# Kernel tuning notes

Measured on AMD Instinct MI355X. Metric: run time of the kernel, lower is better.

The kernel has to match this reference:

```python
import math
import jax, jax.numpy as jnp
import numpy as np

B, N, C = 4, 2048, 256
KMAX, RATIO, ITERS, H = 1024, 12.0, 3, 4
TAU, SIG_FLOOR, INIT_SIG_MIX, INIT_OFF, JIT = 1.0, 0.03, 0.1, 0.5, 1e-6
W_KL, W_ENT, W_OCC, W_COL = 0.05, 0.0, 0.5, 0.1
K_USE = min(max(1, math.ceil(N / RATIO)), KMAX)  # 171
EPS = 1e-8


def _sym(M):
    return 0.5 * (M + jnp.swapaxes(M, -1, -2))


def _l2n(x):
    return x / jnp.maximum(jnp.linalg.norm(x, axis=-1, keepdims=True), 1e-12)


def _ln(x, g, b):
    m = x.mean(-1, keepdims=True)
    v = ((x - m) ** 2).mean(-1, keepdims=True)
    return (x - m) / jnp.sqrt(v + 1e-5) * g + b


def setup_inputs():
    key = jax.random.key(0)
    ks = jax.random.split(key, 16)
    s = jax.random.normal(ks[0], (B, N, C), jnp.float32)
    mu = jax.random.normal(ks[1], (B, N, 3), jnp.float32)
    # per-point SPD covariances (Sigma must be PSD for the overlap solve)
    L = jax.random.normal(ks[2], (B, N, 3, 3), jnp.float32) * 0.3
    Sigma = L @ jnp.swapaxes(L, -1, -2) + 0.05 * jnp.eye(3, dtype=jnp.float32)
    mask = jnp.ones((B, N), jnp.float32)
    lim = 1.0 / math.sqrt(C)
    u = lambda k, sh: jax.random.uniform(k, sh, jnp.float32, -lim, lim)
    return dict(
        s=s, mu=mu, Sigma=Sigma, mask=mask,
        slot_embed_pool=jax.random.normal(ks[3], (KMAX, C), jnp.float32) * 0.02,
        geo_offsets_pool=jax.random.normal(ks[4], (KMAX, 3), jnp.float32) * 0.5,
        gating_W=u(ks[5], (C, C)), proj_q_W=u(ks[6], (C, C)), proj_k_W=u(ks[7], (C, C)),
        gru_w_ih=u(ks[8], (3 * C, C)), gru_w_hh=u(ks[9], (3 * C, C)),
        gru_b_ih=u(ks[10], (3 * C,)), gru_b_hh=u(ks[11], (3 * C,)),
        ln_g=jnp.ones((C,), jnp.float32), ln_b=jnp.zeros((C,), jnp.float32),
        mlp_w1=u(ks[12], (4 * C, C)), mlp_b1=u(ks[13], (4 * C,)),
        mlp_w2=u(ks[14], (C, 4 * C)), mlp_b2=u(ks[15], (C,)),
        w_geo=jnp.float32(1.0),
        geo_scale_raw=jnp.full((H,), -4.0, jnp.float32),
        geo_bias=jnp.full((H,), -6.0, jnp.float32),
    )


def _forward(s, mu, Sigma, mask, slot_embed_pool, geo_offsets_pool, gating_W,
             proj_q_W, proj_k_W, gru_w_ih, gru_w_hh, gru_b_ih, gru_b_hh,
             ln_g, ln_b, mlp_w1, mlp_b1, mlp_w2, mlp_b2,
             w_geo, geo_scale_raw, geo_bias):
    I3 = jnp.eye(3, dtype=s.dtype)
    m1 = mask[:, :, None]                    # [B,N,1]
    cnt = jnp.maximum(mask.sum(1), EPS)      # [B]

    # ---- slot selection (eval mode: no gate noise, rand_slots=0) ----
    s_global = (s * m1).sum(1) / cnt[:, None]
    q = _l2n(s_global @ gating_W.T)
    kn = _l2n(slot_embed_pool)
    scores = q @ kn.T                        # [B,KMAX]
    idx = jax.lax.top_k(scores, K_USE)[1]    # [B,K]
    slots = slot_embed_pool[idx]             # [B,K,C]
    geo_off = geo_offsets_pool[idx]          # [B,K,3]

    # ---- masked mean/std of mu ----
    mean = (mu * m1).sum(1) / cnt[:, None]   # [B,3]
    dm = mu - mean[:, None, :]
    cov = jnp.einsum('bni,bnj->bij', dm * m1, dm) / cnt[:, None, None]
    cov = _sym(cov)
    std = jnp.sqrt(jnp.maximum(jnp.diagonal(cov, axis1=-2, axis2=-1), EPS))
    std = jnp.maximum(std, SIG_FLOOR)
    mu_k = mean[:, None, :] + geo_off * (INIT_OFF * std[:, None, :])

    Sig_avg = _sym((Sigma * m1[..., None]).sum(1) / cnt[:, None, None])
    Sig_k = jnp.broadcast_to(Sig_avg[:, None] * INIT_SIG_MIX, (B, K_USE, 3, 3))
    Sig_k = Sig_k + (SIG_FLOOR ** 2) * I3 + JIT * I3

    k_sem = s @ proj_k_W.T                   # [B,N,C]
    a_h = jax.nn.softplus(geo_scale_raw)     # [H]
    A = None
    for _ in range(ITERS):
        q_sem = slots @ proj_q_W.T           # [B,K,C]
        logits_sem = jnp.einsum('bnc,bkc->bnk', k_sem, q_sem) / math.sqrt(C)
        delta = mu[:, :, None, :] - mu_k[:, None, :, :]       # [B,N,K,3]
        sig_sum = Sigma[:, :, None] + Sig_k[:, None]          # [B,N,K,3,3]
        sol = jnp.linalg.solve(sig_sum, delta[..., None])[..., 0]
        maha = (delta * sol).sum(-1)
        logdet = jnp.linalg.slogdet(sig_sum)[1]
        G = -0.5 * (maha + logdet)                            # [B,N,K]
        geo = (a_h[None, :, None, None] * G[:, None] + geo_bias[None, :, None, None]).sum(1)
        logits = (logits_sem + w_geo * geo) / max(TAU, 1e-6)
        logits = jnp.where(m1 < 0.5, -1e9, logits)
        A = jax.nn.softmax(logits, axis=-1) * m1              # [B,N,K]
        # moment-matching merge (A already mask-weighted; matches torch A*mask)
        occ = jnp.maximum(A.sum(1), EPS)                      # [B,K]
        mu_k = jnp.einsum('bnk,bni->bki', A, mu) / occ[..., None]
        d = mu[:, :, None, :] - mu_k[:, None, :, :]
        outer = d[..., :, None] * d[..., None, :]             # [B,N,K,3,3]
        Sig_k = (jnp.einsum('bnk,bnij->bkij', A, Sigma)
                 + jnp.einsum('bnk,bnkij->bkij', A, outer)) / occ[:, :, None, None]
        Sig_k = _sym(Sig_k) + max(JIT, 1e-6) * I3
        dg = jnp.diagonal(Sig_k, axis1=-2, axis2=-1)
        dg_f = jnp.maximum(dg, SIG_FLOOR ** 2)
        Sig_k = Sig_k - I3 * dg[..., None, :] + I3 * dg_f[..., None, :]
        Sig_k = _sym(Sig_k) + JIT * I3
        denom = jnp.maximum(A.sum(1), 1e-8)
        slot_in = jnp.einsum('bnk,bnc->bkc', A, s) / denom[..., None]
        # GRU cell
        x = slot_in.reshape(-1, C)
        h = slots.reshape(-1, C)
        gi = x @ gru_w_ih.T + gru_b_ih
        gh = h @ gru_w_hh.T + gru_b_hh
        r = jax.nn.sigmoid(gi[:, :C] + gh[:, :C])
        z = jax.nn.sigmoid(gi[:, C:2 * C] + gh[:, C:2 * C])
        n = jnp.tanh(gi[:, 2 * C:] + r * gh[:, 2 * C:])
        slots = ((1.0 - z) * n + z * h).reshape(B, K_USE, C)
        xm = _ln(slots, ln_g, ln_b)
        slots = slots + (jax.nn.gelu(xm @ mlp_w1.T + mlp_b1, approximate=False) @ mlp_w2.T + mlp_b2)

    # ---- losses ----
    hist = jnp.zeros((KMAX,), jnp.float32).at[idx.reshape(-1)].add(1.0)
    p = hist / jnp.maximum(hist.sum(), 1.0)
    pc = jnp.maximum(p, 1e-8)
    usage_kl = (pc * (jnp.log(pc) - math.log(1.0 / KMAX))).sum()
    usage_neg_ent = (pc * jnp.log(pc)).sum()
    occ2 = (A * m1).sum(1)
    occ2 = occ2 / jnp.maximum(occ2.sum(-1, keepdims=True), 1e-8)
    occ_mse = ((occ2 - 1.0 / K_USE) ** 2).mean()
    X = jnp.swapaxes(A * m1, 1, 2)           # [B,K,N]
    Xn = X / jnp.maximum(jnp.linalg.norm(X, axis=-1, keepdims=True), 1e-8)
    Gm = jnp.einsum('bkn,bln->bkl', Xn, Xn)
    eyeK = jnp.eye(K_USE, dtype=A.dtype)[None]
    off = (Gm - eyeK) * (1.0 - eyeK)
    col = (off ** 2).mean()
    total = W_KL * usage_kl + W_ENT * usage_neg_ent + W_OCC * occ_mse + W_COL * col
    return (A, slots, mu_k, Sig_k, idx, usage_kl, usage_neg_ent, occ_mse, col, total)


def reference(s, mu, Sigma, mask, slot_embed_pool, geo_offsets_pool, gating_W,
              proj_q_W, proj_k_W, gru_w_ih, gru_w_hh, gru_b_ih, gru_b_hh,
              ln_g, ln_b, mlp_w1, mlp_b1, mlp_w2, mlp_b2,
              w_geo, geo_scale_raw, geo_bias):
    return _forward(s, mu, Sigma, mask, slot_embed_pool, geo_offsets_pool, gating_W,
                    proj_q_W, proj_k_W, gru_w_ih, gru_w_hh, gru_b_ih, gru_b_hh,
                    ln_g, ln_b, mlp_w1, mlp_b1, mlp_w2, mlp_b2,
                    w_geo, geo_scale_raw, geo_bias)
```

## Files before the change

kernel.cpp:

```cpp
#include <hip/hip_runtime.h>
#include <math.h>

#define B_ 4
#define N_ 2048
#define C_ 256
#define KMAX_ 1024
#define KU_ 171
#define BK_ 684
#define ITERS_ 3
#define H_ 4
#define EPS_ 1e-8f
#define SIGF_ 0.03f
#define JIT_ 1e-6f
#define LOGKMAX_ 6.93147180559945f

#define WS_CNT 0
#define WS_MUS 4
#define WS_MOS 16
#define WS_SGS 40
#define WS_COLACC 100
#define WS_SSUM 128
#define WS_STATS_BYTES (1152*4)
#define WS_MEAN 1152
#define WS_STD 1164
#define WS_SIGAVG 1176
#define WS_IDXI 1216
#define WS_KSEM 1920
#define WS_QSEM (WS_KSEM+2097152)
#define WS_OCC  (WS_QSEM+175104)
#define WS_PART (WS_OCC+704)
#define WS_W2P  WS_PART
#define WS_GBUF (WS_PART+1400832)
#define WS_ATA  WS_GBUF
#define WS_SNEW (WS_GBUF+700416)
#define WS_HID  (WS_SNEW+175104)
#define WS_ACPART (WS_HID+700416)
#define WS_QV   (WS_ACPART+28160)
#define WS_SCORE (WS_QV+1024)

#define O_A 0
#define O_SLOTS 1400832
#define O_MUK   1575936
#define O_SIGK  1577988
#define O_IDX   1584144
#define O_KL    1584828
#define O_ENT   1584829
#define O_OCC   1584830
#define O_COL   1584831
#define O_TOT   1584832

__device__ __forceinline__ float wred(float v) {
  #pragma unroll
  for (int i = 32; i; i >>= 1) v += __shfl_xor(v, i);
  return v;
}
__device__ __forceinline__ float wmax(float v) {
  #pragma unroll
  for (int i = 32; i; i >>= 1) v = fmaxf(v, __shfl_xor(v, i));
  return v;
}

__device__ __forceinline__ float blk_red(float v, float* red, int t) {
  red[t] = v; __syncthreads();
  #pragma unroll
  for (int s = 128; s > 0; s >>= 1) {
    if (t < s) red[t] += red[t + s];
    __syncthreads();
  }
  float r = red[0]; __syncthreads();
  return r;
}

__global__ __launch_bounds__(256) void k_stats(const float* __restrict__ s,
    const float* __restrict__ mu, const float* __restrict__ Sigma,
    const float* __restrict__ mask, float* __restrict__ ws) {
  int blk = blockIdx.x; int b = blk / 8; int nc = blk % 8; int t = threadIdx.x;
  int n = nc * 256 + t;
  float m = mask[b * N_ + n];
  const float* mun = mu + ((size_t)(b * N_ + n)) * 3;
  float m0 = mun[0], m1v = mun[1], m2 = mun[2];
  const float* sgn = Sigma + ((size_t)(b * N_ + n)) * 9;
  float sg[9];
  #pragma unroll
  for (int j = 0; j < 9; j++) sg[j] = sgn[j];
  int lane = t & 63;
  float vals[19];
  vals[0] = m; vals[1] = m * m0; vals[2] = m * m1v; vals[3] = m * m2;
  vals[4] = m * m0 * m0; vals[5] = m * m0 * m1v; vals[6] = m * m0 * m2;
  vals[7] = m * m1v * m1v; vals[8] = m * m1v * m2; vals[9] = m * m2 * m2;
  #pragma unroll
  for (int j = 0; j < 9; j++) vals[10 + j] = m * sg[j];
  #pragma unroll
  for (int j = 0; j < 19; j++) {
    float v = wred(vals[j]);
    if (lane == 0) {
      int base = (j == 0) ? WS_CNT + b : (j < 4 ? WS_MUS + b * 3 + (j - 1)
                 : (j < 10 ? WS_MOS + b * 6 + (j - 4) : WS_SGS + b * 9 + (j - 10)));
      atomicAdd(ws + base, v);
    }
  }
  const float* sb = s + ((size_t)b * N_ + nc * 256) * C_;
  const float* mk = mask + b * N_ + nc * 256;
  float sa = 0.f;
  #pragma unroll 4
  for (int nn = 0; nn < 256; nn++) sa += mk[nn] * sb[(size_t)nn * C_ + t];
  atomicAdd(ws + WS_SSUM + b * C_ + t, sa);
}

__global__ __launch_bounds__(256) void k_qv(float* __restrict__ ws,
    const float* __restrict__ gW, float* __restrict__ qv_o) {
  int b = blockIdx.x, t = threadIdx.x;
  __shared__ float sb[C_];
  __shared__ float rv[256];
  sb[t] = ws[WS_SSUM + b * C_ + t];
  __syncthreads();
  if (blockIdx.x == 0 && t < B_) {
    int bb = t;
    float cnt = fmaxf(ws[WS_CNT + bb], EPS_);
    float me[3];
    #pragma unroll
    for (int i = 0; i < 3; i++) { me[i] = ws[WS_MUS + bb * 3 + i] / cnt; ws[WS_MEAN + bb * 3 + i] = me[i]; }
    const int dg[3] = {0, 3, 5};
    #pragma unroll
    for (int i = 0; i < 3; i++) {
      float cov = ws[WS_MOS + bb * 6 + dg[i]] / cnt - me[i] * me[i];
      ws[WS_STD + bb * 3 + i] = fmaxf(sqrtf(fmaxf(cov, EPS_)), SIGF_);
    }
    #pragma unroll
    for (int i = 0; i < 3; i++)
      #pragma unroll
      for (int j = 0; j < 3; j++)
        ws[WS_SIGAVG + bb * 9 + i * 3 + j] =
            0.5f * (ws[WS_SGS + bb * 9 + i * 3 + j] + ws[WS_SGS + bb * 9 + j * 3 + i]) / cnt;
  }
  const float4* g4 = (const float4*)(gW + (size_t)t * C_);
  float qr = 0.f;
  #pragma unroll 4
  for (int c4 = 0; c4 < 64; c4++) {
    float4 g = g4[c4];
    qr += sb[c4 * 4] * g.x + sb[c4 * 4 + 1] * g.y + sb[c4 * 4 + 2] * g.z + sb[c4 * 4 + 3] * g.w;
  }
  float n2 = blk_red(qr * qr, rv, t);
  qv_o[b * C_ + t] = qr / fmaxf(sqrtf(n2), 1e-12f);
}

__global__ __launch_bounds__(256) void k_score(const float* __restrict__ qv,
    const float* __restrict__ pool, float* __restrict__ score) {
  int blk = blockIdx.x; int b = blk >> 4; int pc = blk & 15;
  int t = threadIdx.x; int row = pc * 64 + (t >> 2); int q = t & 3;
  __shared__ float qs[C_];
  qs[t] = qv[b * C_ + t];
  __syncthreads();
  const float4* p4 = (const float4*)(pool + (size_t)row * C_ + q * 64);
  float d = 0.f, p2 = 0.f;
  #pragma unroll
  for (int i = 0; i < 16; i++) {
    float4 pv = p4[i];
    int c = q * 64 + i * 4;
    d += qs[c] * pv.x + qs[c + 1] * pv.y + qs[c + 2] * pv.z + qs[c + 3] * pv.w;
    p2 += pv.x * pv.x + pv.y * pv.y + pv.z * pv.z + pv.w * pv.w;
  }
  d += __shfl_xor(d, 1); d += __shfl_xor(d, 2);
  p2 += __shfl_xor(p2, 1); p2 += __shfl_xor(p2, 2);
  if (q == 0) score[b * KMAX_ + row] = d / fmaxf(sqrtf(p2), 1e-12f);
}

__global__ __launch_bounds__(256) void k_sort(const float* __restrict__ score,
    int* __restrict__ idx_o, float* __restrict__ idxf_o) {
  int b = blockIdx.x, t = threadIdx.x;
  __shared__ float val[KMAX_]; __shared__ int id[KMAX_];
  for (int j = t; j < KMAX_; j += 256) { val[j] = score[b * KMAX_ + j]; id[j] = j; }
  __syncthreads();
  for (int kk = 2; kk <= KMAX_; kk <<= 1) {
    for (int j = kk >> 1; j > 0; j >>= 1) {
      for (int i = t; i < KMAX_; i += 256) {
        int ix = i ^ j;
        if (ix > i) {
          float va = val[i], vb = val[ix]; int ia = id[i], ib = id[ix];
          bool bBeforeA = (vb > va) || (vb == va && ib < ia);
          bool up = ((i & kk) == 0);
          if (up == bBeforeA) {
            val[i] = vb; val[ix] = va; id[i] = ib; id[ix] = ia;
          }
        }
      }
      __syncthreads();
    }
  }
  if (t < KU_) {
    idx_o[b * KU_ + t] = id[t];
    idxf_o[b * KU_ + t] = (float)id[t];
  }
}

__global__ __launch_bounds__(256) void k_init(const int* __restrict__ idx,
    const float* __restrict__ pool, const float* __restrict__ geop,
    const float* __restrict__ ws, float* __restrict__ slots,
    float* __restrict__ mu_k, float* __restrict__ sig_k) {
  int blk = blockIdx.x; int b = blk / KU_, k = blk % KU_; int t = threadIdx.x;
  int j = idx[b * KU_ + k];
  slots[((size_t)(b * KU_ + k)) * C_ + t] = pool[(size_t)j * C_ + t];
  if (t < 3) {
    mu_k[(b * KU_ + k) * 3 + t] = ws[WS_MEAN + b * 3 + t] + geop[j * 3 + t] * (0.5f * ws[WS_STD + b * 3 + t]);
  }
  if (t < 9) {
    float v = ws[WS_SIGAVG + b * 9 + t] * 0.1f;
    if (t == 0 || t == 4 || t == 8) v += SIGF_ * SIGF_ + JIT_;
    sig_k[((size_t)(b * KU_ + k)) * 9 + t] = v;
  }
}

template<int ROWS>
__global__ __launch_bounds__(256) void k_gemm_plain(const float* __restrict__ in,
    const float* __restrict__ W, float* __restrict__ out, int IN, int OUT, float scale) {
  extern __shared__ float sm[];
  int t = threadIdx.x; int r0 = blockIdx.x * ROWS;
  int C4 = IN >> 2;
  for (int i = t; i < ROWS * C4; i += 256) {
    int rr = i / C4;
    ((float4*)sm)[i] = ((const float4*)(in + (size_t)(r0 + rr) * IN))[i - rr * C4];
  }
  __syncthreads();
  const float4* W4 = (const float4*)(W + (size_t)t * IN);
  const float4* sm4 = (const float4*)sm;
  float acc[ROWS];
  #pragma unroll
  for (int a = 0; a < ROWS; a++) acc[a] = 0.f;
  for (int c4 = 0; c4 < C4; c4++) {
    float4 wv = W4[c4];
    #pragma unroll
    for (int a = 0; a < ROWS; a++) {
      float4 sv = sm4[a * C4 + c4];
      acc[a] += sv.x * wv.x + sv.y * wv.y + sv.z * wv.z + sv.w * wv.w;
    }
  }
  #pragma unroll
  for (int a = 0; a < ROWS; a++)
    out[(size_t)(r0 + a) * OUT + t] = acc[a] * scale;
}

#define LG_R 8
__global__ __launch_bounds__(256) void k_lgsm(const float* __restrict__ ksem,
    const float* __restrict__ qsem, const float* __restrict__ mu,
    const float* __restrict__ Sigma, const float* __restrict__ mask,
    const float* __restrict__ mu_k, const float* __restrict__ sig_k,
    const float* __restrict__ wgeo, const float* __restrict__ gsr,
    const float* __restrict__ gbias, float* __restrict__ A) {
  __shared__ float ksm[LG_R * C_];
  __shared__ float Asm[LG_R][172];
  __shared__ float muk[KU_ * 3];
  __shared__ float sgk[KU_ * 6];
  __shared__ float rowd[LG_R][10];
  int blk = blockIdx.x; int b = blk / (N_ / LG_R); int nt = blk % (N_ / LG_R);
  int t = threadIdx.x; int r0 = nt * LG_R;
  for (int i = t; i < LG_R * (C_ >> 2); i += 256) {
    int rr = i >> 6;
    ((float4*)ksm)[i] = ((const float4*)(ksem + ((size_t)(b * N_ + r0 + rr)) * C_))[i & 63];
  }
  for (int i = t; i < KU_ * 3; i += 256) muk[i] = mu_k[(size_t)b * KU_ * 3 + i];
  for (int i = t; i < KU_ * 6; i += 256) {
    int k = i / 6, c = i % 6;
    const int map[6] = {0, 1, 2, 4, 5, 8};
    sgk[i] = sig_k[((size_t)(b * KU_ + k)) * 9 + map[c]];
  }
  if (t < LG_R * 10) {
    int rr = t / 10, c = t % 10;
    int n = r0 + rr;
    float v;
    if (c == 0) v = mask[b * N_ + n];
    else if (c < 4) v = mu[((size_t)(b * N_ + n)) * 3 + (c - 1)];
    else {
      const int map[6] = {0, 1, 2, 4, 5, 8};
      v = Sigma[((size_t)(b * N_ + n)) * 9 + map[c - 4]];
    }
    rowd[rr][c] = v;
  }
  __syncthreads();
  if (t < KU_) {
    const float4* q4 = (const float4*)(qsem + ((size_t)(b * KU_ + t)) * C_);
    const float4* sm4 = (const float4*)ksm;
    float acc[LG_R];
    #pragma unroll
    for (int a = 0; a < LG_R; a++) acc[a] = 0.f;
    for (int c4 = 0; c4 < 64; c4++) {
      float4 qv = q4[c4];
      #pragma unroll
      for (int a = 0; a < LG_R; a++) {
        float4 sv = sm4[a * 64 + c4];
        acc[a] += sv.x * qv.x + sv.y * qv.y + sv.z * qv.z + sv.w * qv.w;
      }
    }
    float ah = 0.f, bs = 0.f;
    #pragma unroll
    for (int h = 0; h < H_; h++) {
      float x = gsr[h];
      ah += fmaxf(x, 0.f) + log1pf(expf(-fabsf(x)));
      bs += gbias[h];
    }
    float wg = wgeo[0];
    float mk0 = muk[t * 3], mk1 = muk[t * 3 + 1], mk2 = muk[t * 3 + 2];
    float k00 = sgk[t * 6], k01 = sgk[t * 6 + 1], k02 = sgk[t * 6 + 2];
    float k11 = sgk[t * 6 + 3], k12 = sgk[t * 6 + 4], k22 = sgk[t * 6 + 5];
    #pragma unroll
    for (int a = 0; a < LG_R; a++) {
      float m = rowd[a][0];
      float d0 = rowd[a][1] - mk0, d1 = rowd[a][2] - mk1, d2 = rowd[a][3] - mk2;
      float s00 = rowd[a][4] + k00, s01 = rowd[a][5] + k01, s02 = rowd[a][6] + k02;
      float s11 = rowd[a][7] + k11, s12 = rowd[a][8] + k12, s22 = rowd[a][9] + k22;
      float c00 = s11 * s22 - s12 * s12;
      float c01 = s02 * s12 - s01 * s22;
      float c02 = s01 * s12 - s02 * s11;
      float det = s00 * c00 + s01 * c01 + s02 * c02;
      float c11 = s00 * s22 - s02 * s02;
      float c12 = s01 * s02 - s00 * s12;
      float c22 = s00 * s11 - s01 * s01;
      float inv = 1.0f / det;
      float x0 = (c00 * d0 + c01 * d1 + c02 * d2) * inv;
      float x1 = (c01 * d0 + c11 * d1 + c12 * d2) * inv;
      float x2 = (c02 * d0 + c12 * d1 + c22 * d2) * inv;
      float maha = d0 * x0 + d1 * x1 + d2 * x2;
      float logdet = logf(fmaxf(det, 1e-30f));
      float G = -0.5f * (maha + logdet);
      float l = acc[a] * 0.0625f + wg * (ah * G + bs);
      if (m < 0.5f) l = -1e9f;
      Asm[a][t] = l;
    }
  }
  __syncthreads();
  int w = t >> 6, lane = t & 63;
  #pragma unroll
  for (int q = 0; q < 2; q++) {
    int a = w * 2 + q;
    float v0 = (lane < KU_) ? Asm[a][lane] : -INFINITY;
    float v1 = (lane + 64 < KU_) ? Asm[a][lane + 64] : -INFINITY;
    float v2 = (lane + 128 < KU_) ? Asm[a][lane + 128] : -INFINITY;
    float mx = wmax(fmaxf(v0, fmaxf(v1, v2)));
    float e0 = (lane < KU_) ? expf(v0 - mx) : 0.f;
    float e1 = (lane + 64 < KU_) ? expf(v1 - mx) : 0.f;
    float e2 = (lane + 128 < KU_) ? expf(v2 - mx) : 0.f;
    float ss = wred(e0 + e1 + e2);
    float scale = rowd[a][0] / ss;
    if (lane < KU_) Asm[a][lane] = e0 * scale;
    if (lane + 64 < KU_) Asm[a][lane + 64] = e1 * scale;
    if (lane + 128 < KU_) Asm[a][lane + 128] = e2 * scale;
  }
  __syncthreads();
  for (int i = t; i < LG_R * KU_; i += 256) {
    int a = i / KU_, k = i - a * KU_;
    A[((size_t)(b * N_ + r0 + a)) * KU_ + k] = Asm[a][k];
  }
}

#define AC_NC 4
__global__ __launch_bounds__(256) void k_amoms(const float* __restrict__ A,
    const float* __restrict__ mu, const float* __restrict__ Sigma,
    const float* __restrict__ s, float* __restrict__ acpart,
    float* __restrict__ atpart) {
  __shared__ float shm[1024];
  __shared__ float red2[4][16][10];
  int t = threadIdx.x;
  if (blockIdx.x < 176) {
    int blk = blockIdx.x;
    int nc = blk & 3; int tmp = blk >> 2; int kt = tmp % 11; int b = tmp / 11;
    int nn = t >> 4; int kk = t & 15;
    int k = kt * 16 + kk;
    float S[10];
    #pragma unroll
    for (int i = 0; i < 10; i++) S[i] = 0.f;
    float (*rowd)[10] = (float(*)[10])shm;
    const int NCH = N_ / AC_NC;
    for (int n0 = nc * NCH; n0 < nc * NCH + NCH; n0 += 16) {
      __syncthreads();
      if (t < 144) {
        int rr = t / 9, c = t % 9;
        int n = n0 + rr;
        float v;
        if (c < 3) v = mu[((size_t)(b * N_ + n)) * 3 + c];
        else {
          const int map[6] = {0, 1, 2, 4, 5, 8};
          v = Sigma[((size_t)(b * N_ + n)) * 9 + map[c - 3]];
        }
        rowd[rr][c] = v;
      }
      float a = (k < KU_) ? A[((size_t)(b * N_ + n0 + nn)) * KU_ + k] : 0.f;
      __syncthreads();
      float m0 = rowd[nn][0], m1 = rowd[nn][1], m2 = rowd[nn][2];
      float g0 = rowd[nn][3], g1 = rowd[nn][4], g2 = rowd[nn][5];
      float g4 = rowd[nn][6], g5 = rowd[nn][7], g8 = rowd[nn][8];
      S[0] += a; S[1] += a * m0; S[2] += a * m1; S[3] += a * m2;
      S[4] += a * (g0 + m0 * m0); S[5] += a * (g1 + m0 * m1); S[6] += a * (g2 + m0 * m2);
      S[7] += a * (g4 + m1 * m1); S[8] += a * (g5 + m1 * m2); S[9] += a * (g8 + m2 * m2);
    }
    #pragma unroll
    for (int i = 0; i < 10; i++) { S[i] += __shfl_xor(S[i], 16); S[i] += __shfl_xor(S[i], 32); }
    int w = t >> 6, lane = t & 63;
    if (lane < 16) {
      #pragma unroll
      for (int i = 0; i < 10; i++) red2[w][lane][i] = S[i];
    }
    __syncthreads();
    if (t < 160) {
      int k2 = t / 10, i = t % 10;
      float v = red2[0][k2][i] + red2[1][k2][i] + red2[2][k2][i] + red2[3][k2][i];
      acpart[(((size_t)nc * B_ + b) * 176 + kt * 16 + k2) * 10 + i] = v;
    }
  } else {
    int blk = blockIdx.x - 176;
    int nc = blk & 7; int tmp = blk >> 3; int kt = tmp % 11; int b = tmp / 11;
    int k0 = kt * 16;
    float* Ach = shm;
    float acc[16];
    #pragma unroll
    for (int j = 0; j < 16; j++) acc[j] = 0.f;
    for (int n0 = nc * 256; n0 < nc * 256 + 256; n0 += 64) {
      __syncthreads();
      for (int i = t; i < 64 * 16; i += 256) {
        int nn = i >> 4, kk = i & 15; int k = k0 + kk;
        Ach[i] = (k < KU_) ? A[((size_t)(b * N_ + n0 + nn)) * KU_ + k] : 0.f;
      }
      __syncthreads();
      for (int nn = 0; nn < 64; nn++) {
        float xv = s[((size_t)(b * N_ + n0 + nn)) * C_ + t];
        #pragma unroll
        for (int j = 0; j < 16; j++) acc[j] += Ach[(nn << 4) + j] * xv;
      }
    }
    #pragma unroll
    for (int j = 0; j < 16; j++) {
      int k = k0 + j;
      if (k < KU_) atpart[((size_t)nc * (B_ * BK_ / 4) + b * KU_ + k) * C_ + t] = acc[j];
    }
  }
}

__global__ __launch_bounds__(256) void k_gg(const float* __restrict__ atpart,
    const float* __restrict__ acpart, const float* __restrict__ slots,
    const float* __restrict__ wih, const float* __restrict__ bih,
    const float* __restrict__ whh, const float* __restrict__ bhh,
    float* __restrict__ gbuf, float* __restrict__ occ,
    float* __restrict__ mu_k, float* __restrict__ sig_k) {
  int t = threadIdx.x;
  if (blockIdx.x >= 86) {
    if (blockIdx.y != 0) return;
    int i = (blockIdx.x - 86) * 256 + t;
    if (i >= B_ * KU_) return;
    int b = i / KU_, k = i % KU_;
    float p[10];
    #pragma unroll
    for (int j = 0; j < 10; j++) {
      float v = 0.f;
      #pragma unroll
      for (int nc = 0; nc < AC_NC; nc++)
        v += acpart[(((size_t)nc * B_ + b) * 176 + k) * 10 + j];
      p[j] = v;
    }
    float o = p[0];
    occ[b * KU_ + k] = o;
    float oc = fmaxf(o, EPS_);
    float s1x = p[1], s1y = p[2], s1z = p[3];
    float q0 = s1x / oc, q1 = s1y / oc, q2 = s1z / oc;
    mu_k[(b * KU_ + k) * 3 + 0] = q0;
    mu_k[(b * KU_ + k) * 3 + 1] = q1;
    mu_k[(b * KU_ + k) * 3 + 2] = q2;
    float v00 = (p[4] - 2.f * q0 * s1x + o * q0 * q0) / oc + JIT_;
    float v01 = (p[5] - q0 * s1y - s1x * q1 + o * q0 * q1) / oc;
    float v02 = (p[6] - q0 * s1z - s1x * q2 + o * q0 * q2) / oc;
    float v11 = (p[7] - 2.f * q1 * s1y + o * q1 * q1) / oc + JIT_;
    float v12 = (p[8] - q1 * s1z - s1y * q2 + o * q1 * q2) / oc;
    float v22 = (p[9] - 2.f * q2 * s1z + o * q2 * q2) / oc + JIT_;
    v00 = fmaxf(v00, SIGF_ * SIGF_) + JIT_;
    v11 = fmaxf(v11, SIGF_ * SIGF_) + JIT_;
    v22 = fmaxf(v22, SIGF_ * SIGF_) + JIT_;
    float* po = sig_k + ((size_t)(b * KU_ + k)) * 9;
    po[0] = v00; po[1] = v01; po[2] = v02;
    po[3] = v01; po[4] = v11; po[5] = v12;
    po[6] = v02; po[7] = v12; po[8] = v22;
    return;
  }
  int p = blockIdx.y; int r0 = blockIdx.x * 8;
  __shared__ float sx[8 * C_];
  __shared__ float sh[8 * C_];
  __shared__ float socc[8];
  bool needx = (p < 3), needh = (p != 2);
  if (t < 8) {
    int r = r0 + t;
    float o = 0.f;
    if (r < BK_) {
      int b = r / KU_, k = r % KU_;
      #pragma unroll
      for (int nc = 0; nc < AC_NC; nc++)
        o += acpart[(((size_t)nc * B_ + b) * 176 + k) * 10];
    }
    socc[t] = fmaxf(o, 1e-8f);
  }
  __syncthreads();
  for (int i = t; i < 8 * C_; i += 256) {
    int rr = i >> 8, c = i & 255;
    int r = r0 + rr;
    if (r < BK_) {
      if (needx) {
        float v = 0.f;
        #pragma unroll
        for (int nc = 0; nc < 8; nc++) v += atpart[((size_t)nc * BK_ + r) * C_ + c];
        sx[i] = v / socc[rr];
      }
      if (needh) sh[i] = slots[(size_t)r * C_ + c];
    } else {
      if (needx) sx[i] = 0.f;
      if (needh) sh[i] = 0.f;
    }
  }
  __syncthreads();
  int grow = (p >= 2) ? 512 + t : p * 256 + t;
  float acc[8];
  #pragma unroll
  for (int a = 0; a < 8; a++) acc[a] = 0.f;
  const float4* sx4 = (const float4*)sx;
  const float4* sh4 = (const float4*)sh;
  if (p < 2) {
    const float4* wi = (const float4*)(wih + (size_t)grow * C_);
    const float4* wh = (const float4*)(whh + (size_t)grow * C_);
    for (int c4 = 0; c4 < 64; c4++) {
      float4 a1 = wi[c4], a2 = wh[c4];
      #pragma unroll
      for (int a = 0; a < 8; a++) {
        float4 xv = sx4[a * 64 + c4], hv = sh4[a * 64 + c4];
        acc[a] += xv.x * a1.x + xv.y * a1.y + xv.z * a1.z + xv.w * a1.w
                + hv.x * a2.x + hv.y * a2.y + hv.z * a2.z + hv.w * a2.w;
      }
    }
  } else if (p == 2) {
    const float4* wi = (const float4*)(wih + (size_t)grow * C_);
    for (int c4 = 0; c4 < 64; c4++) {
      float4 a1 = wi[c4];
      #pragma unroll
      for (int a = 0; a < 8; a++) {
        float4 xv = sx4[a * 64 + c4];
        acc[a] += xv.x * a1.x + xv.y * a1.y + xv.z * a1.z + xv.w * a1.w;
      }
    }
  } else {
    const float4* wh = (const float4*)(whh + (size_t)grow * C_);
    for (int c4 = 0; c4 < 64; c4++) {
      float4 a2 = wh[c4];
      #pragma unroll
      for (int a = 0; a < 8; a++) {
        float4 hv = sh4[a * 64 + c4];
        acc[a] += hv.x * a2.x + hv.y * a2.y + hv.z * a2.z + hv.w * a2.w;
      }
    }
  }
  float bias = (p < 2) ? (bih[grow] + bhh[grow]) : ((p == 2) ? bih[grow] : bhh[grow]);
  #pragma unroll
  for (int a = 0; a < 8; a++) {
    int r = r0 + a;
    if (r < BK_) gbuf[((size_t)p * BK_ + r) * C_ + t] = acc[a] + bias;
  }
}

__global__ __launch_bounds__(256) void k_w1ln(const float* __restrict__ gbuf,
    const float* __restrict__ slots, const float* __restrict__ lng,
    const float* __restrict__ lnb, const float* __restrict__ w1p,
    const float* __restrict__ b1p, float* __restrict__ snew,
    float* __restrict__ hid) {
  int r0 = blockIdx.x * 4; int t = threadIdx.x; int oc = blockIdx.y * 256 + t;
  __shared__ float ssn[4 * C_];
  __shared__ float sxm[4 * C_];
  bool wr = (blockIdx.y == 0);
  for (int i = t; i < 4 * C_; i += 256) {
    int rr = i >> 8, c = i & 255;
    int r = r0 + rr;
    float gr = gbuf[((size_t)0 * BK_ + r) * C_ + c];
    float gz = gbuf[((size_t)1 * BK_ + r) * C_ + c];
    float gi = gbuf[((size_t)2 * BK_ + r) * C_ + c];
    float gh = gbuf[((size_t)3 * BK_ + r) * C_ + c];
    float rg = 1.f / (1.f + expf(-gr));
    float z = 1.f / (1.f + expf(-gz));
    float n = tanhf(gi + rg * gh);
    float h = slots[(size_t)r * C_ + c];
    float sn = (1.f - z) * n + z * h;
    ssn[i] = sn;
    if (wr) snew[(size_t)r * C_ + c] = sn;
  }
// ... 94 lines not shown
  int nc = blk & 7; int tmp = blk >> 3; int kt = tmp % 11; int b = tmp / 11;
  int t = threadIdx.x; int k0 = kt * 16;
  __shared__ float Ach[64 * 16];
  float acc[16];
  #pragma unroll
  for (int j = 0; j < 16; j++) acc[j] = 0.f;
  for (int n0 = nc * 256; n0 < nc * 256 + 256; n0 += 64) {
    __syncthreads();
    for (int i = t; i < 64 * 16; i += 256) {
      int nn = i >> 4, kk = i & 15; int k = k0 + kk;
      Ach[i] = (k < KU_) ? A[((size_t)(b * N_ + n0 + nn)) * KU_ + k] : 0.f;
    }
    __syncthreads();
    if (t < NX) {
      for (int nn = 0; nn < 64; nn++) {
        float xv = X[((size_t)(b * N_ + n0 + nn)) * NX + t];
        #pragma unroll
        for (int j = 0; j < 16; j++) acc[j] += Ach[(nn << 4) + j] * xv;
      }
    }
  }
  if (t < NX) {
    #pragma unroll
    for (int j = 0; j < 16; j++) {
      int k = k0 + j;
      if (k < KU_) atomicAdd(&out[((size_t)(b * KU_ + k)) * NX + t], acc[j]);
    }
  }
}

__global__ __launch_bounds__(256) void k_histocc(const int* __restrict__ idx,
    const float* __restrict__ occ, float* __restrict__ okl,
    float* __restrict__ oent, float* __restrict__ oocc) {
  int t = threadIdx.x;
  __shared__ float buf[KMAX_];
  __shared__ float red[256];
  if (blockIdx.x == 0) {
    for (int i = t; i < KMAX_; i += 256) buf[i] = 0.f;
    __syncthreads();
    for (int i = t; i < B_ * KU_; i += 256) atomicAdd(&buf[idx[i]], 1.0f);
    __syncthreads();
    float kl = 0.f, ent = 0.f;
    const float tot = (float)(B_ * KU_);
    for (int i = t; i < KMAX_; i += 256) {
      float pc = fmaxf(buf[i] / tot, 1e-8f);
      float lp = logf(pc);
      kl += pc * (lp + LOGKMAX_);
      ent += pc * lp;
    }
    kl = blk_red(kl, red, t); ent = blk_red(ent, red, t);
    if (t == 0) { okl[0] = kl; oent[0] = ent; }
  } else {
    for (int i = t; i < B_ * KU_; i += 256) buf[i] = occ[i];
    __syncthreads();
    __shared__ float bsum[B_];
    for (int b = 0; b < B_; b++) {
      float s = 0.f;
      for (int i = t; i < KU_; i += 256) s += buf[b * KU_ + i];
      s = blk_red(s, red, t);
      if (t == 0) bsum[b] = fmaxf(s, 1e-8f);
      __syncthreads();
    }
    float acc = 0.f;
    const float invK = 1.0f / (float)KU_;
    for (int i = t; i < B_ * KU_; i += 256) {
      int b = i / KU_;
      float v = buf[i] / bsum[b] - invK;
      acc += v * v;
    }
    acc = blk_red(acc, red, t);
    if (t == 0) oocc[0] = acc / (float)(B_ * KU_);
  }
}

__global__ __launch_bounds__(256) void k_colpart(const float* __restrict__ AtA,
    float* __restrict__ colacc) {
  int blk = blockIdx.x; int b = blk / KU_, k = blk % KU_; int t = threadIdx.x;
  float acc = 0.f;
  if (t < KU_ && t != k) {
    float dk = AtA[((size_t)(b * KU_ + k)) * KU_ + k];
    float dt = AtA[((size_t)(b * KU_ + t)) * KU_ + t];
    float v  = AtA[((size_t)(b * KU_ + k)) * KU_ + t];
    float gm = v / (fmaxf(sqrtf(dk), 1e-8f) * fmaxf(sqrtf(dt), 1e-8f));
    acc = gm * gm;
  }
  float v = wred(acc);
  __shared__ float p[4];
  if ((t & 63) == 0) p[t >> 6] = v;
  __syncthreads();
  if (t == 0) atomicAdd(colacc, p[0] + p[1] + p[2] + p[3]);
}

__global__ void k_colfin(const float* __restrict__ colacc,
    const float* __restrict__ okl, const float* __restrict__ oent,
    const float* __restrict__ oocc, float* __restrict__ ocol, float* __restrict__ otot) {
  float col = colacc[0] / (float)(B_ * KU_ * KU_);
  ocol[0] = col;
  otot[0] = 0.05f * okl[0] + 0.0f * oent[0] + 0.5f * oocc[0] + 0.1f * col;
}

extern "C" void kernel_launch(void* const* d_in, const int* in_sizes, int n_in,
                              void* d_out_v, int out_size, void* d_ws, size_t ws_size,
                              hipStream_t stream) {
  const float* s     = (const float*)d_in[0];
  const float* mu    = (const float*)d_in[1];
  const float* Sigma = (const float*)d_in[2];
  const float* mask  = (const float*)d_in[3];
  const float* pool  = (const float*)d_in[4];
  const float* geop  = (const float*)d_in[5];
  const float* gW    = (const float*)d_in[6];
  const float* qW    = (const float*)d_in[7];
  const float* kW    = (const float*)d_in[8];
  const float* wih   = (const float*)d_in[9];
  const float* whh   = (const float*)d_in[10];
  const float* bih   = (const float*)d_in[11];
  const float* bhh   = (const float*)d_in[12];
  const float* lng   = (const float*)d_in[13];
  const float* lnb   = (const float*)d_in[14];
  const float* w1    = (const float*)d_in[15];
  const float* b1    = (const float*)d_in[16];
  const float* w2    = (const float*)d_in[17];
  const float* b2    = (const float*)d_in[18];
  const float* wgeo  = (const float*)d_in[19];
  const float* gsr   = (const float*)d_in[20];
  const float* gbias = (const float*)d_in[21];

  float* out = (float*)d_out_v;
  float* A     = out + O_A;
  float* slots = out + O_SLOTS;
  float* muk   = out + O_MUK;
  float* sigk  = out + O_SIGK;
  float* idxf  = out + O_IDX;
  float* okl   = out + O_KL;
  float* oent  = out + O_ENT;
  float* oocc  = out + O_OCC;
  float* ocol  = out + O_COL;
  float* otot  = out + O_TOT;

  float* ws = (float*)d_ws;
  int*   idxi   = (int*)(ws + WS_IDXI);
  float* ksem   = ws + WS_KSEM;
  float* qsem   = ws + WS_QSEM;
  float* occ    = ws + WS_OCC;
  float* atpart = ws + WS_PART;
  float* gbuf   = ws + WS_GBUF;
  float* snew   = ws + WS_SNEW;
  float* hid    = ws + WS_HID;
  float* w2part = ws + WS_W2P;
  float* acpart = ws + WS_ACPART;
  float* ata    = ws + WS_ATA;
  float* colacc = ws + WS_COLACC;

  hipMemsetAsync(ws, 0, WS_STATS_BYTES, stream);
  k_stats<<<B_ * 8, 256, 0, stream>>>(s, mu, Sigma, mask, ws);
  k_qv<<<B_, 256, 0, stream>>>(ws, gW, ws + WS_QV);
  k_score<<<B_ * 16, 256, 0, stream>>>(ws + WS_QV, pool, ws + WS_SCORE);
  k_sort<<<B_, 256, 0, stream>>>(ws + WS_SCORE, idxi, idxf);
  k_init<<<B_ * KU_, 256, 0, stream>>>(idxi, pool, geop, ws, slots, muk, sigk);

  k_gemm_plain<8><<<1024, 256, 8 * C_ * 4, stream>>>(s, kW, ksem, C_, C_, 1.0f);
  k_gemm_plain<4><<<171, 256, 4 * C_ * 4, stream>>>(slots, qW, qsem, C_, C_, 1.0f);

  for (int it = 0; it < ITERS_; ++it) {
    k_lgsm<<<B_ * (N_ / LG_R), 256, 0, stream>>>(ksem, qsem, mu, Sigma, mask,
                                                 muk, sigk, wgeo, gsr, gbias, A);
    k_amoms<<<176 + 352, 256, 0, stream>>>(A, mu, Sigma, s, acpart, atpart);
    k_gg<<<dim3(89, 4), 256, 0, stream>>>(atpart, acpart, slots, wih, bih, whh, bhh,
                                          gbuf, occ, muk, sigk);
    k_w1ln<<<dim3(171, 4), 256, 0, stream>>>(gbuf, slots, lng, lnb, w1, b1, snew, hid);
    k_w2p<<<dim3(171, 4), 256, 0, stream>>>(hid, w2, w2part);
    k_qsemf<<<171, 256, 0, stream>>>(snew, w2part, b2, qW, slots, qsem);
  }

  hipMemsetAsync(ata, 0, (size_t)B_ * KU_ * KU_ * 4, stream);
  k_atn<<<B_ * 11 * 8, 256, 0, stream>>>(A, A, ata, KU_);
  k_colpart<<<B_ * KU_, 256, 0, stream>>>(ata, colacc);
  k_histocc<<<2, 256, 0, stream>>>(idxi, occ, okl, oent, oocc);
  k_colfin<<<1, 1, 0, stream>>>(colacc, okl, oent, oocc, ocol, otot);
}
```

Measured before the change: 786.5 us.

## Register-tile projection GEMMs and logit kernel; split stats into separate kernels

Replaces the per-thread single-output-column GEMM with a 32-row register-tiled kernel where each thread computes 8 rows by 4 columns. The logit/softmax kernel now handles 32 rows per block, with each thread covering 8 rows by 3 slots. Before, only 171 of 256 threads did work in that kernel. The s-row summation moves out of the stats kernel into a wider grid so it no longer runs serially over 256 rows per thread. The aim is to cut weight reloads and raise utilisation, at the cost of more registers and shared memory and fewer blocks for the logit kernel.

```diff
diff --git a/kernel.cpp b/kernel.cpp
--- a/kernel.cpp
+++ b/kernel.cpp
@@ -71,9 +71,9 @@
   return r;
 }
 
-__global__ __launch_bounds__(256) void k_stats(const float* __restrict__ s,
-    const float* __restrict__ mu, const float* __restrict__ Sigma,
-    const float* __restrict__ mask, float* __restrict__ ws) {
+__global__ __launch_bounds__(256) void k_mom(const float* __restrict__ mu,
+    const float* __restrict__ Sigma, const float* __restrict__ mask,
+    float* __restrict__ ws) {
   int blk = blockIdx.x; int b = blk / 8; int nc = blk % 8; int t = threadIdx.x;
   int n = nc * 256 + t;
   float m = mask[b * N_ + n];
@@ -99,11 +99,16 @@
       atomicAdd(ws + base, v);
     }
   }
-  const float* sb = s + ((size_t)b * N_ + nc * 256) * C_;
-  const float* mk = mask + b * N_ + nc * 256;
+}
+
+__global__ __launch_bounds__(256) void k_ssum(const float* __restrict__ s,
+    const float* __restrict__ mask, float* __restrict__ ws) {
+  int blk = blockIdx.x; int b = blk / 64; int nc = blk % 64; int t = threadIdx.x;
+  const float* sb = s + ((size_t)b * N_ + nc * 32) * C_;
+  const float* mk = mask + b * N_ + nc * 32;
   float sa = 0.f;
-  #pragma unroll 4
-  for (int nn = 0; nn < 256; nn++) sa += mk[nn] * sb[(size_t)nn * C_ + t];
+  #pragma unroll 8
+  for (int nn = 0; nn < 32; nn++) sa += mk[nn] * sb[(size_t)nn * C_ + t];
   atomicAdd(ws + WS_SSUM + b * C_ + t, sa);
 }
 
@@ -210,50 +215,66 @@
   }
 }
 
-template<int ROWS>
-__global__ __launch_bounds__(256) void k_gemm_plain(const float* __restrict__ in,
-    const float* __restrict__ W, float* __restrict__ out, int IN, int OUT, float scale) {
-  extern __shared__ float sm[];
-  int t = threadIdx.x; int r0 = blockIdx.x * ROWS;
-  int C4 = IN >> 2;
-  for (int i = t; i < ROWS * C4; i += 256) {
-    int rr = i / C4;
-    ((float4*)sm)[i] = ((const float4*)(in + (size_t)(r0 + rr) * IN))[i - rr * C4];
-  }
-  __syncthreads();
-  const float4* W4 = (const float4*)(W + (size_t)t * IN);
+__global__ __launch_bounds__(256) void k_gemm32(const float* __restrict__ in,
+    const float* __restrict__ W, float* __restrict__ out, int R) {
+  __shared__ float sm[32 * C_];
+  int t = threadIdx.x; int r0 = blockIdx.x * 32;
+  for (int i = t; i < 32 * 64; i += 256) {
+    int rr = i >> 6; int r = r0 + rr;
+    float4 v = {0.f, 0.f, 0.f, 0.f};
+    if (r < R) v = ((const float4*)(in + (size_t)r * C_))[i & 63];
+    ((float4*)sm)[i] = v;
+  }
+  __syncthreads();
+  int cg = t & 63, rg = t >> 6;
+  const float4* w0 = (const float4*)(W + (size_t)cg * C_);
+  const float4* w1 = (const float4*)(W + (size_t)(cg + 64) * C_);
+  const float4* w2 = (const float4*)(W + (size_t)(cg + 128) * C_);
+  const float4* w3 = (const float4*)(W + (size_t)(cg + 192) * C_);
   const float4* sm4 = (const float4*)sm;
-  float acc[ROWS];
-  #pragma unroll
-  for (int a = 0; a < ROWS; a++) acc[a] = 0.f;
-  for (int c4 = 0; c4 < C4; c4++) {
-    float4 wv = W4[c4];
-    #pragma unroll
-    for (int a = 0; a < ROWS; a++) {
-      float4 sv = sm4[a * C4 + c4];
-      acc[a] += sv.x * wv.x + sv.y * wv.y + sv.z * wv.z + sv.w * wv.w;
-    }
-  }
-  #pragma unroll
-  for (int a = 0; a < ROWS; a++)
-    out[(size_t)(r0 + a) * OUT + t] = acc[a] * scale;
-}
-
-#define LG_R 8
+  float acc[8][4];
+  #pragma unroll
+  for (int a = 0; a < 8; a++)
+    #pragma unroll
+    for (int j = 0; j < 4; j++) acc[a][j] = 0.f;
+  for (int c4 = 0; c4 < 64; c4++) {
+    float4 a0 = w0[c4], a1 = w1[c4], a2 = w2[c4], a3 = w3[c4];
+    #pragma unroll
+    for (int a = 0; a < 8; a++) {
+      float4 sv = sm4[(rg * 8 + a) * 64 + c4];
+      acc[a][0] += sv.x * a0.x + sv.y * a0.y + sv.z * a0.z + sv.w * a0.w;
+      acc[a][1] += sv.x * a1.x + sv.y * a1.y + sv.z * a1.z + sv.w * a1.w;
+      acc[a][2] += sv.x * a2.x + sv.y * a2.y + sv.z * a2.z + sv.w * a2.w;
+      acc[a][3] += sv.x * a3.x + sv.y * a3.y + sv.z * a3.z + sv.w * a3.w;
+    }
+  }
+  #pragma unroll
+  for (int a = 0; a < 8; a++) {
+    int r = r0 + rg * 8 + a;
+    if (r < R) {
+      out[(size_t)r * C_ + cg]       = acc[a][0];
+      out[(size_t)r * C_ + cg + 64]  = acc[a][1];
+      out[(size_t)r * C_ + cg + 128] = acc[a][2];
+      out[(size_t)r * C_ + cg + 192] = acc[a][3];
+    }
+  }
+}
+
+#define LG32 32
 __global__ __launch_bounds__(256) void k_lgsm(const float* __restrict__ ksem,
     const float* __restrict__ qsem, const float* __restrict__ mu,
     const float* __restrict__ Sigma, const float* __restrict__ mask,
     const float* __restrict__ mu_k, const float* __restrict__ sig_k,
     const float* __restrict__ wgeo, const float* __restrict__ gsr,
     const float* __restrict__ gbias, float* __restrict__ A) {
-  __shared__ float ksm[LG_R * C_];
-  __shared__ float Asm[LG_R][172];
+  __shared__ float ksm[LG32 * C_];
+  __shared__ float Asm[LG32][176];
   __shared__ float muk[KU_ * 3];
   __shared__ float sgk[KU_ * 6];
-  __shared__ float rowd[LG_R][10];
-  int blk = blockIdx.x; int b = blk / (N_ / LG_R); int nt = blk % (N_ / LG_R);
-  int t = threadIdx.x; int r0 = nt * LG_R;
-  for (int i = t; i < LG_R * (C_ >> 2); i += 256) {
+  __shared__ float rowd[LG32][10];
+  int blk = blockIdx.x; int b = blk / (N_ / LG32); int nt = blk % (N_ / LG32);
+  int t = threadIdx.x; int r0 = nt * LG32;
+  for (int i = t; i < LG32 * 64; i += 256) {
     int rr = i >> 6;
     ((float4*)ksm)[i] = ((const float4*)(ksem + ((size_t)(b * N_ + r0 + rr)) * C_))[i & 63];
   }
@@ -263,8 +284,8 @@
     const int map[6] = {0, 1, 2, 4, 5, 8};
     sgk[i] = sig_k[((size_t)(b * KU_ + k)) * 9 + map[c]];
   }
-  if (t < LG_R * 10) {
-    int rr = t / 10, c = t % 10;
+  for (int i = t; i < LG32 * 10; i += 256) {
+    int rr = i / 10, c = i % 10;
     int n = r0 + rr;
     float v;
     if (c == 0) v = mask[b * N_ + n];
@@ -276,37 +297,49 @@
     rowd[rr][c] = v;
   }
   __syncthreads();
-  if (t < KU_) {
-    const float4* q4 = (const float4*)(qsem + ((size_t)(b * KU_ + t)) * C_);
-    const float4* sm4 = (const float4*)ksm;
-    float acc[LG_R];
-    #pragma unroll
-    for (int a = 0; a < LG_R; a++) acc[a] = 0.f;
-    for (int c4 = 0; c4 < 64; c4++) {
-      float4 qv = q4[c4];
-      #pragma unroll
-      for (int a = 0; a < LG_R; a++) {
-        float4 sv = sm4[a * 64 + c4];
-        acc[a] += sv.x * qv.x + sv.y * qv.y + sv.z * qv.z + sv.w * qv.w;
-      }
-    }
-    float ah = 0.f, bs = 0.f;
-    #pragma unroll
-    for (int h = 0; h < H_; h++) {
-      float x = gsr[h];
-      ah += fmaxf(x, 0.f) + log1pf(expf(-fabsf(x)));
-      bs += gbias[h];
-    }
-    float wg = wgeo[0];
-    float mk0 = muk[t * 3], mk1 = muk[t * 3 + 1], mk2 = muk[t * 3 + 2];
-    float k00 = sgk[t * 6], k01 = sgk[t * 6 + 1], k02 = sgk[t * 6 + 2];
-    float k11 = sgk[t * 6 + 3], k12 = sgk[t * 6 + 4], k22 = sgk[t * 6 + 5];
-    #pragma unroll
-    for (int a = 0; a < LG_R; a++) {
-      float m = rowd[a][0];
-      float d0 = rowd[a][1] - mk0, d1 = rowd[a][2] - mk1, d2 = rowd[a][3] - mk2;
-      float s00 = rowd[a][4] + k00, s01 = rowd[a][5] + k01, s02 = rowd[a][6] + k02;
-      float s11 = rowd[a][7] + k11, s12 = rowd[a][8] + k12, s22 = rowd[a][9] + k22;
+  int kg = t & 63, rg = t >> 6;
+  int k0i = kg, k1i = kg + 64, k2i = kg + 128;
+  bool v2 = (k2i < KU_);
+  const float* qbase = qsem + (size_t)b * KU_ * C_;
+  const float4* q0 = (const float4*)(qbase + (size_t)k0i * C_);
+  const float4* q1 = (const float4*)(qbase + (size_t)k1i * C_);
+  const float4* q2 = (const float4*)(qbase + (size_t)(v2 ? k2i : k0i) * C_);
+  const float4* sm4 = (const float4*)ksm;
+  float acc[8][3];
+  #pragma unroll
+  for (int a = 0; a < 8; a++) { acc[a][0] = 0.f; acc[a][1] = 0.f; acc[a][2] = 0.f; }
+  for (int c4 = 0; c4 < 64; c4++) {
+    float4 qa = q0[c4], qb = q1[c4], qc = q2[c4];
+    #pragma unroll
+    for (int a = 0; a < 8; a++) {
+      float4 sv = sm4[(rg * 8 + a) * 64 + c4];
+      acc[a][0] += sv.x * qa.x + sv.y * qa.y + sv.z * qa.z + sv.w * qa.w;
+      acc[a][1] += sv.x * qb.x + sv.y * qb.y + sv.z * qb.z + sv.w * qb.w;
+      acc[a][2] += sv.x * qc.x + sv.y * qc.y + sv.z * qc.z + sv.w * qc.w;
+    }
+  }
+  float ah = 0.f, bs = 0.f;
+  #pragma unroll
+  for (int h = 0; h < H_; h++) {
+    float x = gsr[h];
+    ah += fmaxf(x, 0.f) + log1pf(expf(-fabsf(x)));
+    bs += gbias[h];
+  }
+  float wg = wgeo[0];
+  #pragma unroll
+  for (int kk = 0; kk < 3; kk++) {
+    int k = kg + kk * 64;
+    if (kk == 2 && !v2) break;
+    float mk0 = muk[k * 3], mk1 = muk[k * 3 + 1], mk2 = muk[k * 3 + 2];
+    float s0 = sgk[k * 6], s1 = sgk[k * 6 + 1], s2 = sgk[k * 6 + 2];
+    float s3 = sgk[k * 6 + 3], s4 = sgk[k * 6 + 4], s5 = sgk[k * 6 + 5];
+    #pragma unroll
+    for (int a = 0; a < 8; a++) {
+      int row = rg * 8 + a;
+      float m = rowd[row][0];
+      float d0 = rowd[row][1] - mk0, d1 = rowd[row][2] - mk1, d2 = rowd[row][3] - mk2;
+      float s00 = rowd[row][4] + s0, s01 = rowd[row][5] + s1, s02 = rowd[row][6] + s2;
+      float s11 = rowd[row][7] + s3, s12 = rowd[row][8] + s4, s22 = rowd[row][9] + s5;
       float c00 = s11 * s22 - s12 * s12;
       float c01 = s02 * s12 - s01 * s22;
       float c02 = s01 * s12 - s02 * s11;
@@ -321,23 +354,23 @@
       float maha = d0 * x0 + d1 * x1 + d2 * x2;
       float logdet = logf(fmaxf(det, 1e-30f));
       float G = -0.5f * (maha + logdet);
-      float l = acc[a] * 0.0625f + wg * (ah * G + bs);
+      float l = acc[a][kk] * 0.0625f + wg * (ah * G + bs);
       if (m < 0.5f) l = -1e9f;
-      Asm[a][t] = l;
+      Asm[row][k] = l;
     }
   }
   __syncthreads();
   int w = t >> 6, lane = t & 63;
   #pragma unroll
-  for (int q = 0; q < 2; q++) {
-    int a = w * 2 + q;
+  for (int q = 0; q < 8; q++) {
+    int a = w * 8 + q;
     float v0 = (lane < KU_) ? Asm[a][lane] : -INFINITY;
     float v1 = (lane + 64 < KU_) ? Asm[a][lane + 64] : -INFINITY;
-    float v2 = (lane + 128 < KU_) ? Asm[a][lane + 128] : -INFINITY;
-    float mx = wmax(fmaxf(v0, fmaxf(v1, v2)));
+    float vv2 = (lane + 128 < KU_) ? Asm[a][lane + 128] : -INFINITY;
+    float mx = wmax(fmaxf(v0, fmaxf(v1, vv2)));
     float e0 = (lane < KU_) ? expf(v0 - mx) : 0.f;
     float e1 = (lane + 64 < KU_) ? expf(v1 - mx) : 0.f;
-    float e2 = (lane + 128 < KU_) ? expf(v2 - mx) : 0.f;
+    float e2 = (lane + 128 < KU_) ? expf(vv2 - mx) : 0.f;
     float ss = wred(e0 + e1 + e2);
     float scale = rowd[a][0] / ss;
     if (lane < KU_) Asm[a][lane] = e0 * scale;
@@ -345,7 +378,7 @@
     if (lane + 128 < KU_) Asm[a][lane + 128] = e2 * scale;
   }
   __syncthreads();
-  for (int i = t; i < LG_R * KU_; i += 256) {
+  for (int i = t; i < LG32 * KU_; i += 256) {
     int a = i / KU_, k = i - a * KU_;
     A[((size_t)(b * N_ + r0 + a)) * KU_ + k] = Asm[a][k];
   }
@@ -428,7 +461,7 @@
     #pragma unroll
     for (int j = 0; j < 16; j++) {
       int k = k0 + j;
-      if (k < KU_) atpart[((size_t)nc * (B_ * BK_ / 4) + b * KU_ + k) * C_ + t] = acc[j];
+      if (k < KU_) atpart[((size_t)nc * (B_ * KU_) + b * KU_ + k) * C_ + t] = acc[j];
     }
   }
 }
@@ -829,17 +862,18 @@
   float* colacc = ws + WS_COLACC;
 
   hipMemsetAsync(ws, 0, WS_STATS_BYTES, stream);
-  k_stats<<<B_ * 8, 256, 0, stream>>>(s, mu, Sigma, mask, ws);
+  k_mom<<<B_ * 8, 256, 0, stream>>>(mu, Sigma, mask, ws);
+  k_ssum<<<B_ * 64, 256, 0, stream>>>(s, mask, ws);
   k_qv<<<B_, 256, 0, stream>>>(ws, gW, ws + WS_QV);
   k_score<<<B_ * 16, 256, 0, stream>>>(ws + WS_QV, pool, ws + WS_SCORE);
   k_sort<<<B_, 256, 0, stream>>>(ws + WS_SCORE, idxi, idxf);
   k_init<<<B_ * KU_, 256, 0, stream>>>(idxi, pool, geop, ws, slots, muk, sigk);
 
-  k_gemm_plain<8><<<1024, 256, 8 * C_ * 4, stream>>>(s, kW, ksem, C_, C_, 1.0f);
-  k_gemm_plain<4><<<171, 256, 4 * C_ * 4, stream>>>(slots, qW, qsem, C_, C_, 1.0f);
+  k_gemm32<<<(B_ * N_) / 32, 256, 0, stream>>>(s, kW, ksem, B_ * N_);
+  k_gemm32<<<(BK_ + 31) / 32, 256, 0, stream>>>(slots, qW, qsem, BK_);
 
   for (int it = 0; it < ITERS_; ++it) {
-    k_lgsm<<<B_ * (N_ / LG_R), 256, 0, stream>>>(ksem, qsem, mu, Sigma, mask,
+    k_lgsm<<<B_ * (N_ / LG32), 256, 0, stream>>>(ksem, qsem, mu, Sigma, mask,
                                                  muk, sigk, wgeo, gsr, gbias, A);
     k_amoms<<<176 + 352, 256, 0, stream>>>(A, mu, Sigma, s, acpart, atpart);
     k_gg<<<dim3(89, 4), 256, 0, stream>>>(atpart, acpart, slots, wih, bih, whh, bhh,
```

Result: slower. 811.2 us (+3.1%).

## Split stats kernel and use register-tiled 32-row GEMM for key/query projections

Applied to the files above, without the earlier changes.

The stats kernel is split into a moments kernel and a separate masked feature-sum kernel. The sum kernel runs over 256 blocks instead of 32, so more of the GPU works on the column reduction. Both one-shot projection GEMMs now use a kernel that tiles 32 rows per block, with each thread computing 8 rows by 4 output columns, to reuse weight loads across rows. This adds more atomics and an extra launch, and raises register use per thread. The atpart index also changes from BK_/4 to KU_, which looks like an equivalent cleanup.

```diff
diff --git a/kernel.cpp b/kernel.cpp
--- a/kernel.cpp
+++ b/kernel.cpp
@@ -71,9 +71,9 @@
   return r;
 }
 
-__global__ __launch_bounds__(256) void k_stats(const float* __restrict__ s,
-    const float* __restrict__ mu, const float* __restrict__ Sigma,
-    const float* __restrict__ mask, float* __restrict__ ws) {
+__global__ __launch_bounds__(256) void k_mom(const float* __restrict__ mu,
+    const float* __restrict__ Sigma, const float* __restrict__ mask,
+    float* __restrict__ ws) {
   int blk = blockIdx.x; int b = blk / 8; int nc = blk % 8; int t = threadIdx.x;
   int n = nc * 256 + t;
   float m = mask[b * N_ + n];
@@ -99,11 +99,16 @@
       atomicAdd(ws + base, v);
     }
   }
-  const float* sb = s + ((size_t)b * N_ + nc * 256) * C_;
-  const float* mk = mask + b * N_ + nc * 256;
+}
+
+__global__ __launch_bounds__(256) void k_ssum(const float* __restrict__ s,
+    const float* __restrict__ mask, float* __restrict__ ws) {
+  int blk = blockIdx.x; int b = blk / 64; int nc = blk % 64; int t = threadIdx.x;
+  const float* sb = s + ((size_t)b * N_ + nc * 32) * C_;
+  const float* mk = mask + b * N_ + nc * 32;
   float sa = 0.f;
-  #pragma unroll 4
-  for (int nn = 0; nn < 256; nn++) sa += mk[nn] * sb[(size_t)nn * C_ + t];
+  #pragma unroll 8
+  for (int nn = 0; nn < 32; nn++) sa += mk[nn] * sb[(size_t)nn * C_ + t];
   atomicAdd(ws + WS_SSUM + b * C_ + t, sa);
 }
 
@@ -210,33 +215,49 @@
   }
 }
 
-template<int ROWS>
-__global__ __launch_bounds__(256) void k_gemm_plain(const float* __restrict__ in,
-    const float* __restrict__ W, float* __restrict__ out, int IN, int OUT, float scale) {
-  extern __shared__ float sm[];
-  int t = threadIdx.x; int r0 = blockIdx.x * ROWS;
-  int C4 = IN >> 2;
-  for (int i = t; i < ROWS * C4; i += 256) {
-    int rr = i / C4;
-    ((float4*)sm)[i] = ((const float4*)(in + (size_t)(r0 + rr) * IN))[i - rr * C4];
-  }
-  __syncthreads();
-  const float4* W4 = (const float4*)(W + (size_t)t * IN);
+__global__ __launch_bounds__(256) void k_gemm32(const float* __restrict__ in,
+    const float* __restrict__ W, float* __restrict__ out, int R) {
+  __shared__ float sm[32 * C_];
+  int t = threadIdx.x; int r0 = blockIdx.x * 32;
+  for (int i = t; i < 32 * 64; i += 256) {
+    int rr = i >> 6; int r = r0 + rr;
+    float4 v = {0.f, 0.f, 0.f, 0.f};
+    if (r < R) v = ((const float4*)(in + (size_t)r * C_))[i & 63];
+    ((float4*)sm)[i] = v;
+  }
+  __syncthreads();
+  int cg = t & 63, rg = t >> 6;
+  const float4* w0 = (const float4*)(W + (size_t)cg * C_);
+  const float4* w1 = (const float4*)(W + (size_t)(cg + 64) * C_);
+  const float4* w2 = (const float4*)(W + (size_t)(cg + 128) * C_);
+  const float4* w3 = (const float4*)(W + (size_t)(cg + 192) * C_);
   const float4* sm4 = (const float4*)sm;
-  float acc[ROWS];
-  #pragma unroll
-  for (int a = 0; a < ROWS; a++) acc[a] = 0.f;
-  for (int c4 = 0; c4 < C4; c4++) {
-    float4 wv = W4[c4];
-    #pragma unroll
-    for (int a = 0; a < ROWS; a++) {
-      float4 sv = sm4[a * C4 + c4];
-      acc[a] += sv.x * wv.x + sv.y * wv.y + sv.z * wv.z + sv.w * wv.w;
-    }
-  }
-  #pragma unroll
-  for (int a = 0; a < ROWS; a++)
-    out[(size_t)(r0 + a) * OUT + t] = acc[a] * scale;
+  float acc[8][4];
+  #pragma unroll
+  for (int a = 0; a < 8; a++)
+    #pragma unroll
+    for (int j = 0; j < 4; j++) acc[a][j] = 0.f;
+  for (int c4 = 0; c4 < 64; c4++) {
+    float4 a0 = w0[c4], a1 = w1[c4], a2 = w2[c4], a3 = w3[c4];
+    #pragma unroll
+    for (int a = 0; a < 8; a++) {
+      float4 sv = sm4[(rg * 8 + a) * 64 + c4];
+      acc[a][0] += sv.x * a0.x + sv.y * a0.y + sv.z * a0.z + sv.w * a0.w;
+      acc[a][1] += sv.x * a1.x + sv.y * a1.y + sv.z * a1.z + sv.w * a1.w;
+      acc[a][2] += sv.x * a2.x + sv.y * a2.y + sv.z * a2.z + sv.w * a2.w;
+      acc[a][3] += sv.x * a3.x + sv.y * a3.y + sv.z * a3.z + sv.w * a3.w;
+    }
+  }
+  #pragma unroll
+  for (int a = 0; a < 8; a++) {
+    int r = r0 + rg * 8 + a;
+    if (r < R) {
+      out[(size_t)r * C_ + cg]       = acc[a][0];
+      out[(size_t)r * C_ + cg + 64]  = acc[a][1];
+      out[(size_t)r * C_ + cg + 128] = acc[a][2];
+      out[(size_t)r * C_ + cg + 192] = acc[a][3];
+    }
+  }
 }
 
 #define LG_R 8
@@ -428,7 +449,7 @@
     #pragma unroll
     for (int j = 0; j < 16; j++) {
       int k = k0 + j;
-      if (k < KU_) atpart[((size_t)nc * (B_ * BK_ / 4) + b * KU_ + k) * C_ + t] = acc[j];
+      if (k < KU_) atpart[((size_t)nc * (B_ * KU_) + b * KU_ + k) * C_ + t] = acc[j];
     }
   }
 }
@@ -829,14 +850,15 @@
   float* colacc = ws + WS_COLACC;
 
   hipMemsetAsync(ws, 0, WS_STATS_BYTES, stream);
-  k_stats<<<B_ * 8, 256, 0, stream>>>(s, mu, Sigma, mask, ws);
+  k_mom<<<B_ * 8, 256, 0, stream>>>(mu, Sigma, mask, ws);
+  k_ssum<<<B_ * 64, 256, 0, stream>>>(s, mask, ws);
   k_qv<<<B_, 256, 0, stream>>>(ws, gW, ws + WS_QV);
   k_score<<<B_ * 16, 256, 0, stream>>>(ws + WS_QV, pool, ws + WS_SCORE);
   k_sort<<<B_, 256, 0, stream>>>(ws + WS_SCORE, idxi, idxf);
   k_init<<<B_ * KU_, 256, 0, stream>>>(idxi, pool, geop, ws, slots, muk, sigk);
 
-  k_gemm_plain<8><<<1024, 256, 8 * C_ * 4, stream>>>(s, kW, ksem, C_, C_, 1.0f);
-  k_gemm_plain<4><<<171, 256, 4 * C_ * 4, stream>>>(slots, qW, qsem, C_, C_, 1.0f);
+  k_gemm32<<<(B_ * N_) / 32, 256, 0, stream>>>(s, kW, ksem, B_ * N_);
+  k_gemm32<<<(BK_ + 31) / 32, 256, 0, stream>>>(slots, qW, qsem, BK_);
 
   for (int it = 0; it < ITERS_; ++it) {
     k_lgsm<<<B_ * (N_ / LG_R), 256, 0, stream>>>(ksem, qsem, mu, Sigma, mask,
```

Measured after the change: 797.7 us, median of 2. No clear change (+1.4%).
